# Kernel tuning notes

Hardware: AMD Instinct MI355X
Metric: run time of the kernel (lower is better)

Reference implementation:

```python
import jax, jax.numpy as jnp
import numpy as np

# Faithful JAX port of predictTransform: YOLO anchor-box decode.
# prediction: [B, A*(5+C), G, G] raw conv output.
# Returns [B, G*G*A, 5+C] decoded boxes in input-image pixel units.

def setup_inputs() -> dict:
    key = jax.random.key(0)
    B, A, C, IN_DIM, G = 32, 3, 80, 608, 76  # stride = 608 // 76 = 8
    attrs = 5 + C
    prediction = jax.random.normal(key, (B, A * attrs, G, G), dtype=jnp.float32)
    # standard YOLOv3 anchors for the stride-8 head, in input-pixel units
    anchors = jnp.array([[10.0, 13.0], [16.0, 30.0], [33.0, 23.0]], dtype=jnp.float32)
    return {"prediction": prediction, "anchors": anchors, "inputDim": IN_DIM, "numClasses": C}


def reference(prediction, anchors, inputDim, numClasses):
    B = prediction.shape[0]
    stride = inputDim // prediction.shape[2]
    G = inputDim // stride
    A = anchors.shape[0]
    attrs = 5 + numClasses

    # [B, A*attrs, G*G] -> [B, G*G, A*attrs] -> [B, G*G*A, attrs]
    p = prediction.reshape(B, attrs * A, G * G)
    p = jnp.transpose(p, (0, 2, 1)).reshape(B, G * G * A, attrs)

    anc = anchors / stride  # anchors in grid units, [A, 2]

    # grid offsets: np.meshgrid(grid, grid) -> a[i,j]=j (x), b[i,j]=i (y)
    grid = jnp.arange(G, dtype=jnp.float32)
    gx, gy = jnp.meshgrid(grid, grid)  # each [G, G]
    xy = jnp.stack([gx.ravel(), gy.ravel()], axis=-1)        # [G*G, 2]
    xy = jnp.repeat(xy, A, axis=0)[None]                     # [1, G*G*A, 2]
    anc_t = jnp.tile(anc, (G * G, 1))[None]                  # [1, G*G*A, 2]

    txy = jax.nn.sigmoid(p[..., 0:2]) + xy                   # center x,y in grid units
    twh = jnp.exp(p[..., 2:4]) * anc_t                       # w,h in grid units
    conf = jax.nn.sigmoid(p[..., 4:5])                       # objectness
    cls = jax.nn.sigmoid(p[..., 5:])                         # class probs

    boxes = jnp.concatenate([txy, twh], axis=-1) * stride    # back to pixel units
    return jnp.concatenate([boxes, conf, cls], axis=-1)
```

## Files before the change

kernel.cpp:

```cpp
#include <hip/hip_runtime.h>


#define BATCH   32
#define ATTRS   85
#define CH      255
#define G_      76
#define SP      5776
#define STRIDE_F 8.0f
#define S_TILE  64
#define TPB     1024
#define TILES_PER_B 91
#define NTILES  (BATCH * TILES_PER_B)
#define NBLK    512

typedef float f4 __attribute__((ext_vector_type(4)));

__device__ __forceinline__ float decode1(float val, int attr, int s,
                                         float ax, float ay) {
    if (attr == 2) return __expf(val) * ax;
    if (attr == 3) return __expf(val) * ay;
    const float sg = __builtin_amdgcn_rcpf(1.0f + __expf(-val));
    if (attr == 0) return (sg + (float)(s % G_)) * STRIDE_F;
    if (attr == 1) return (sg + (float)(s / G_)) * STRIDE_F;
    return sg;
}

__global__ __launch_bounds__(TPB, 8) void yolo_decode_kernel(
        const float* __restrict__ pred,
        const float* __restrict__ anchors,
        float* __restrict__ out) {
    __shared__ float lds[S_TILE * CH];

    const int tid = threadIdx.x;

    const float a0x = anchors[0], a0y = anchors[1];
    const float a1x = anchors[2], a1y = anchors[3];
    const float a2x = anchors[4], a2y = anchors[5];

    const int c0 = ((tid >> 6) << 2) | (tid & 3);
    const int sl = ((tid >> 2) & 15) << 2;
    const bool act3 = (c0 + 192) < CH;

    const int cA = c0,       aA = cA / ATTRS, atA = cA - aA * ATTRS;
    const int cB = c0 + 64,  aB = cB / ATTRS, atB = cB - aB * ATTRS;
    const int cC = c0 + 128, aC = cC / ATTRS, atC = cC - aC * ATTRS;
    const int cD = c0 + 192, aD = cD / ATTRS, atD = cD - aD * ATTRS;
    const float axA = (aA == 0) ? a0x : (aA == 1) ? a1x : a2x;
    const float ayA = (aA == 0) ? a0y : (aA == 1) ? a1y : a2y;
    const float axB = (aB == 0) ? a0x : (aB == 1) ? a1x : a2x;
    const float ayB = (aB == 0) ? a0y : (aB == 1) ? a1y : a2y;
    const float axC = (aC == 0) ? a0x : (aC == 1) ? a1x : a2x;
    const float ayC = (aC == 0) ? a0y : (aC == 1) ? a1y : a2y;
    const float axD = (aD == 0) ? a0x : (aD == 1) ? a1x : a2x;
    const float ayD = (aD == 0) ? a0y : (aD == 1) ? a1y : a2y;

    int tk = blockIdx.x;
    int b  = tk / TILES_PER_B;
    int t  = tk - b * TILES_PER_B;
    int s0 = t * S_TILE;
    int sw = (t == TILES_PER_B - 1) ? (SP - s0) : S_TILE;
    const float* src = pred + (size_t)b * ((size_t)CH * SP) + s0 + sl;

    f4 v0 = {0,0,0,0}, v1 = {0,0,0,0}, v2 = {0,0,0,0}, v3 = {0,0,0,0};
    if (sl < sw) {
        v0 = *(const f4*)(src + (size_t)cA * SP);
        v1 = *(const f4*)(src + (size_t)cB * SP);
        v2 = *(const f4*)(src + (size_t)cC * SP);
        if (act3) v3 = *(const f4*)(src + (size_t)cD * SP);
    }

    for (;;) {
        const int cb = b, cs0 = s0, csw = sw;

        if (sl < csw) {
            #pragma unroll
            for (int e = 0; e < 4; ++e) {
                const int r = sl + e, s = cs0 + r;
                lds[r * CH + cA] = decode1(v0[e], atA, s, axA, ayA);
                lds[r * CH + cB] = decode1(v1[e], atB, s, axB, ayB);
                lds[r * CH + cC] = decode1(v2[e], atC, s, axC, ayC);
                if (act3) lds[r * CH + cD] = decode1(v3[e], atD, s, axD, ayD);
            }
        }

        const int ntk = tk + NBLK;
        const bool more = (ntk < NTILES);
        if (more) {
            b  = ntk / TILES_PER_B;
            t  = ntk - b * TILES_PER_B;
            s0 = t * S_TILE;
            sw = (t == TILES_PER_B - 1) ? (SP - s0) : S_TILE;
            src = pred + (size_t)b * ((size_t)CH * SP) + s0 + sl;
            if (sl < sw) {
                v0 = *(const f4*)(src + (size_t)cA * SP);
                v1 = *(const f4*)(src + (size_t)cB * SP);
                v2 = *(const f4*)(src + (size_t)cC * SP);
                if (act3) v3 = *(const f4*)(src + (size_t)cD * SP);
            }
        }

        asm volatile("s_waitcnt lgkmcnt(0)" ::: "memory");
        __builtin_amdgcn_sched_barrier(0);
        __builtin_amdgcn_s_barrier();
        __builtin_amdgcn_sched_barrier(0);

        float* __restrict__ dst = out + (size_t)cb * ((size_t)SP * CH)
                                      + (size_t)cs0 * CH;
        const int nf4w = (csw * CH) >> 2;
        for (int j = tid; j < nf4w; j += TPB) {
            f4 w = *(const f4*)(lds + 4 * j);
            __builtin_nontemporal_store(w, (f4*)(dst + 4 * j));
        }

        if (!more) break;

        asm volatile("" ::: "memory");
        __builtin_amdgcn_sched_barrier(0);
        __builtin_amdgcn_s_barrier();
        __builtin_amdgcn_sched_barrier(0);

        tk = ntk;
    }
}

extern "C" void kernel_launch(void* const* d_in, const int* in_sizes, int n_in,
                              void* d_out, int out_size, void* d_ws, size_t ws_size,
                              hipStream_t stream) {
    const float* pred    = (const float*)d_in[0];
    const float* anchors = (const float*)d_in[1];
    float* out = (float*)d_out;

    yolo_decode_kernel<<<NBLK, TPB, 0, stream>>>(pred, anchors, out);
}
```

Measured before the change: 73.15 us.

## Replace persistent tile loop with one block per tile and XCD-aware mapping

Drops the persistent-block loop, which prefetched the next tile's loads before storing the current one. The kernel now launches one block per tile (NTILES blocks) and remaps block IDs so that the tiles of each group of 4 batches land on the same XCD (bid&7). The aim is to remove the loop and barrier overhead and to improve L2 locality per XCD. In exchange it loses the explicit load/store overlap inside a block and relies on hardware scheduling of many blocks instead.

```diff
diff --git a/kernel.cpp b/kernel.cpp
--- a/kernel.cpp
+++ b/kernel.cpp
@@ -11,7 +11,6 @@
 #define TPB     1024
 #define TILES_PER_B 91
 #define NTILES  (BATCH * TILES_PER_B)
-#define NBLK    512
 
 typedef float f4 __attribute__((ext_vector_type(4)));
 
@@ -32,6 +31,14 @@
     __shared__ float lds[S_TILE * CH];
 
     const int tid = threadIdx.x;
+
+    const int bid = blockIdx.x;
+    const int xcd = bid & 7;
+    const int sub = bid >> 3;
+    const int b   = (xcd << 2) + sub / TILES_PER_B;
+    const int t   = sub % TILES_PER_B;
+    const int s0  = t * S_TILE;
+    const int sw  = (t == TILES_PER_B - 1) ? (SP - s0) : S_TILE;
 
     const float a0x = anchors[0], a0y = anchors[1];
     const float a1x = anchors[2], a1y = anchors[3];
@@ -54,13 +61,7 @@
     const float axD = (aD == 0) ? a0x : (aD == 1) ? a1x : a2x;
     const float ayD = (aD == 0) ? a0y : (aD == 1) ? a1y : a2y;
 
-    int tk = blockIdx.x;
-    int b  = tk / TILES_PER_B;
-    int t  = tk - b * TILES_PER_B;
-    int s0 = t * S_TILE;
-    int sw = (t == TILES_PER_B - 1) ? (SP - s0) : S_TILE;
-    const float* src = pred + (size_t)b * ((size_t)CH * SP) + s0 + sl;
-
+    const float* __restrict__ src = pred + (size_t)b * ((size_t)CH * SP) + s0 + sl;
     f4 v0 = {0,0,0,0}, v1 = {0,0,0,0}, v2 = {0,0,0,0}, v3 = {0,0,0,0};
     if (sl < sw) {
         v0 = *(const f4*)(src + (size_t)cA * SP);
@@ -69,57 +70,24 @@
         if (act3) v3 = *(const f4*)(src + (size_t)cD * SP);
     }
 
-    for (;;) {
-        const int cb = b, cs0 = s0, csw = sw;
+    if (sl < sw) {
+        #pragma unroll
+        for (int e = 0; e < 4; ++e) {
+            const int r = sl + e, s = s0 + r;
+            lds[r * CH + cA] = decode1(v0[e], atA, s, axA, ayA);
+            lds[r * CH + cB] = decode1(v1[e], atB, s, axB, ayB);
+            lds[r * CH + cC] = decode1(v2[e], atC, s, axC, ayC);
+            if (act3) lds[r * CH + cD] = decode1(v3[e], atD, s, axD, ayD);
+        }
+    }
+    __syncthreads();
 
-        if (sl < csw) {
-            #pragma unroll
-            for (int e = 0; e < 4; ++e) {
-                const int r = sl + e, s = cs0 + r;
-                lds[r * CH + cA] = decode1(v0[e], atA, s, axA, ayA);
-                lds[r * CH + cB] = decode1(v1[e], atB, s, axB, ayB);
-                lds[r * CH + cC] = decode1(v2[e], atC, s, axC, ayC);
-                if (act3) lds[r * CH + cD] = decode1(v3[e], atD, s, axD, ayD);
-            }
-        }
-
-        const int ntk = tk + NBLK;
-        const bool more = (ntk < NTILES);
-        if (more) {
-            b  = ntk / TILES_PER_B;
-            t  = ntk - b * TILES_PER_B;
-            s0 = t * S_TILE;
-            sw = (t == TILES_PER_B - 1) ? (SP - s0) : S_TILE;
-            src = pred + (size_t)b * ((size_t)CH * SP) + s0 + sl;
-            if (sl < sw) {
-                v0 = *(const f4*)(src + (size_t)cA * SP);
-                v1 = *(const f4*)(src + (size_t)cB * SP);
-                v2 = *(const f4*)(src + (size_t)cC * SP);
-                if (act3) v3 = *(const f4*)(src + (size_t)cD * SP);
-            }
-        }
-
-        asm volatile("s_waitcnt lgkmcnt(0)" ::: "memory");
-        __builtin_amdgcn_sched_barrier(0);
-        __builtin_amdgcn_s_barrier();
-        __builtin_amdgcn_sched_barrier(0);
-
-        float* __restrict__ dst = out + (size_t)cb * ((size_t)SP * CH)
-                                      + (size_t)cs0 * CH;
-        const int nf4w = (csw * CH) >> 2;
-        for (int j = tid; j < nf4w; j += TPB) {
-            f4 w = *(const f4*)(lds + 4 * j);
-            __builtin_nontemporal_store(w, (f4*)(dst + 4 * j));
-        }
-
-        if (!more) break;
-
-        asm volatile("" ::: "memory");
-        __builtin_amdgcn_sched_barrier(0);
-        __builtin_amdgcn_s_barrier();
-        __builtin_amdgcn_sched_barrier(0);
-
-        tk = ntk;
+    float* __restrict__ dst = out + (size_t)b * ((size_t)SP * CH)
+                                  + (size_t)s0 * CH;
+    const int nf4w = (sw * CH) >> 2;
+    for (int j = tid; j < nf4w; j += TPB) {
+        f4 w = *(const f4*)(lds + 4 * j);
+        __builtin_nontemporal_store(w, (f4*)(dst + 4 * j));
     }
 }
 
@@ -130,5 +98,5 @@
     const float* anchors = (const float*)d_in[1];
     float* out = (float*)d_out;
 
-    yolo_decode_kernel<<<NBLK, TPB, 0, stream>>>(pred, anchors, out);
+    yolo_decode_kernel<<<NTILES, TPB, 0, stream>>>(pred, anchors, out);
 }
```

Result: faster. 68.63 us (-6.2%).
